# Kernel tuning notes

Hardware: AMD Instinct MI355X
Metric: run time of the kernel (lower is better)

The kernel has to match this reference:

```python
import jax, jax.numpy as jnp
import numpy as np
from jax import lax

LN_EPS = 1e-5
DENOM_EPS = 1e-6


def taylor_exp(x, f):
    # x: [..., f] -> [..., 1 + f + f*f]
    r2 = np.sqrt(2.0).astype(np.float32)
    rd = np.sqrt(float(f)).astype(np.float32)
    rrd = np.sqrt(np.sqrt(float(f))).astype(np.float32)
    x2 = (x[..., :, None] * x[..., None, :]).reshape(*x.shape[:-1], f * f) / r2
    return jnp.concatenate([jnp.ones_like(x[..., :1]), x / rrd, x2 / rd], axis=-1)


def layer_norm(x, gamma, beta):
    mu = jnp.mean(x, axis=-1, keepdims=True)
    var = jnp.mean(jnp.square(x - mu), axis=-1, keepdims=True)
    return (x - mu) * lax.rsqrt(var + LN_EPS) * gamma + beta


def setup_inputs() -> dict:
    key = jax.random.key(0)
    ks = jax.random.split(key, 24)
    B, L, d, h, f, hd, w = 4, 2048, 1024, 16, 16, 64, 64
    D = 1 + f + f * f  # 273

    def lin_w(k, fi, fo):
        return (jax.random.normal(k, (fi, fo), jnp.float32) / np.sqrt(fi)).astype(jnp.float32)

    def lin_b(k, fo):
        return 0.01 * jax.random.normal(k, (fo,), jnp.float32)

    inp = {
        'x': jax.random.normal(ks[0], (B, L, d), jnp.float32),
        'kv_state': jnp.zeros((B, h, D, hd), jnp.float32),
        'k_state': jnp.zeros((B, h, D), jnp.float32),
        'k_buf': jnp.zeros((1, h, w, hd), jnp.float32),
        'v_buf': jnp.zeros((1, h, w, hd), jnp.float32),
        # LinearAttention projections
        'Wq_lin': lin_w(ks[1], d, f * h), 'bq_lin': lin_b(ks[2], f * h),
        'Wk_lin': lin_w(ks[3], d, f * h), 'bk_lin': lin_b(ks[4], f * h),
        'Wv_lin': lin_w(ks[5], d, hd * h), 'bv_lin': lin_b(ks[6], hd * h),
        'Wo_lin': lin_w(ks[7], d, d), 'bo_lin': lin_b(ks[8], d),
        # BasedBlock window-attention projections
        'Wq': lin_w(ks[9], d, d), 'bq': lin_b(ks[10], d),
        'Wk': lin_w(ks[11], d, d), 'bk': lin_b(ks[12], d),
        'Wv': lin_w(ks[13], d, d), 'bv': lin_b(ks[14], d),
        'Wo': lin_w(ks[15], d, d), 'bo': lin_b(ks[16], d),
        # shared LayerNorm
        'gamma': jnp.ones((d,), jnp.float32),
        'beta': jnp.zeros((d,), jnp.float32),
    }
    return inp


def reference(x, kv_state, k_state, k_buf, v_buf,
              Wq_lin, bq_lin, Wk_lin, bk_lin, Wv_lin, bv_lin, Wo_lin, bo_lin,
              Wq, bq, Wk, bk, Wv, bv, Wo, bo, gamma, beta):
    B, L, d = x.shape
    h = kv_state.shape[1]
    hd = kv_state.shape[3]
    f = Wq_lin.shape[1] // h

    # ---- LinearAttention ----
    q = (x @ Wq_lin + bq_lin).reshape(B, L, h, f).transpose(0, 2, 1, 3)   # b h l f
    k = (x @ Wk_lin + bk_lin).reshape(B, L, h, f).transpose(0, 2, 1, 3)
    v = (x @ Wv_lin + bv_lin).reshape(B, L, h, hd).transpose(0, 2, 1, 3)  # b h l hd
    qf = taylor_exp(q, f)  # b h l D
    kf = taylor_exp(k, f)

    # time-major for scan: [l, b, h, ...]
    qt = qf.transpose(2, 0, 1, 3)
    kt = kf.transpose(2, 0, 1, 3)
    vt = v.transpose(2, 0, 1, 3)

    def step(carry, inp):
        kv, kst = carry
        q_t, k_t, v_t = inp
        kv = kv + k_t[..., :, None] * v_t[..., None, :]            # b h D hd
        kst = kst + k_t                                            # b h D
        num = jnp.einsum('bhd,bhdc->bhc', q_t, kv)
        den = jnp.einsum('bhd,bhd->bh', q_t, kst) + DENOM_EPS
        return (kv, kst), num / den[..., None]

    (kv_new, k_new), outs = lax.scan(step, (kv_state, k_state), (qt, kt, vt))
    lin = outs.transpose(1, 0, 2, 3).reshape(B, L, h * hd)  # b l (h hd)
    lin_out = lin @ Wo_lin + bo_lin  # dropout is identity in eval

    x1 = layer_norm(x + lin_out, gamma, beta)

    # ---- window attention ----
    q2 = (x1 @ Wq + bq).reshape(B, L, h, hd).transpose(0, 2, 1, 3)  # b h l hd
    k2 = (x1 @ Wk + bk).reshape(B, L, h, hd).transpose(0, 2, 1, 3)
    v2 = (x1 @ Wv + bv).reshape(B, L, h, hd).transpose(0, 2, 1, 3)

    new_k = k2[:, :, -1:, :]
    new_v = v2[:, :, -1:, :]
    kb = jnp.broadcast_to(k_buf, (B,) + k_buf.shape[1:])
    vb = jnp.broadcast_to(v_buf, (B,) + v_buf.shape[1:])
    uk = jnp.concatenate([kb[:, :, 1:], new_k], axis=2)  # b h w hd
    uv = jnp.concatenate([vb[:, :, 1:], new_v], axis=2)

    scores = jnp.einsum('bhqd,bhwd->bhqw', q2, uk) / np.sqrt(float(hd))
    attn = jax.nn.softmax(scores, axis=-1)
    win = jnp.einsum('bhqw,bhwd->bhqd', attn, uv)
    win = win.transpose(0, 2, 1, 3).reshape(B, L, h * hd)

    out = layer_norm(x1 + (win @ Wo + bo), gamma, beta)
    return out, kv_new, k_new
```

## Files before the change

kernel.cpp:

```cpp
#include <hip/hip_runtime.h>
#include <math.h>


#define LL 2048
#define DD 1024
#define DFEAT 273
#define NC 16
#define CHUNK 128
#define QKVN 1536

typedef __attribute__((ext_vector_type(8))) short short8;
typedef __attribute__((ext_vector_type(4))) float f32x4;

#define SQ 0.42044820762685725f
#define LF 1.18920711500272107f

__device__ __forceinline__ float4 f4(float a, float b, float c, float d) {
  float4 r; r.x = a; r.y = b; r.z = c; r.w = d; return r;
}

__device__ __forceinline__ unsigned short f2bf(float f) {
  union { float f; unsigned u; } v; v.f = f;
  unsigned r = v.u + 0x7fffu + ((v.u >> 16) & 1u);
  return (unsigned short)(r >> 16);
}

__device__ __forceinline__ float bf2f(unsigned short u) {
  union { unsigned u; float f; } v; v.u = ((unsigned)u) << 16; return v.f;
}

__global__ __launch_bounds__(256) void cast_bf16(
    const float* __restrict__ in, unsigned short* __restrict__ o, int n4) {
  int i = blockIdx.x * 256 + threadIdx.x;
  if (i < n4) {
    float4 v = ((const float4*)in)[i];
    ushort4 r;
    r.x = f2bf(v.x); r.y = f2bf(v.y); r.z = f2bf(v.z); r.w = f2bf(v.w);
    ((ushort4*)o)[i] = r;
  }
}

__global__ __launch_bounds__(256) void castT_all(
    const float* __restrict__ Wql, const float* __restrict__ Wkl,
    const float* __restrict__ Wvl, const float* __restrict__ Wo1,
    const float* __restrict__ Wq2, const float* __restrict__ Wo2,
    const float* __restrict__ bql, const float* __restrict__ bkl,
    const float* __restrict__ bvl,
    unsigned short* __restrict__ Wcomb, unsigned short* __restrict__ WtO1,
    unsigned short* __restrict__ WtQ2, unsigned short* __restrict__ WtO2,
    float* __restrict__ bqkv) {
  __shared__ float t[64][65];
  const int blk = blockIdx.x, tid = threadIdx.x;
  if (blk < 6) {
    int i = blk * 256 + tid;
    float v = (i < 256) ? bql[i] : (i < 512) ? bkl[i - 256] : bvl[i - 512];
    bqkv[i] = v;
  }
  const float* W; unsigned short* Wt; int N, t0;
  if (blk < 64)       { W = Wql; Wt = Wcomb;               N = 256;  t0 = blk; }
  else if (blk < 128) { W = Wkl; Wt = Wcomb + 256 * 1024;  N = 256;  t0 = blk - 64; }
  else if (blk < 384) { W = Wvl; Wt = Wcomb + 512 * 1024;  N = 1024; t0 = blk - 128; }
  else if (blk < 640) { W = Wo1; Wt = WtO1;                N = 1024; t0 = blk - 384; }
  else if (blk < 896) { W = Wq2; Wt = WtQ2;                N = 1024; t0 = blk - 640; }
  else                { W = Wo2; Wt = WtO2;                N = 1024; t0 = blk - 896; }
  const int nt = N >> 6;
  const int k0 = (t0 / nt) * 64, n0 = (t0 % nt) * 64;
#pragma unroll
  for (int p = 0; p < 16; p++) {
    int idx = p * 256 + tid;
    int r = idx >> 6, c = idx & 63;
    t[r][c] = W[(size_t)(k0 + r) * N + n0 + c];
  }
  __syncthreads();
#pragma unroll
  for (int p = 0; p < 16; p++) {
    int idx = p * 256 + tid;
    int rn = idx >> 6, ck = idx & 63;
    Wt[(size_t)(n0 + rn) * 1024 + k0 + ck] = f2bf(t[ck][rn]);
  }
}

__global__ __launch_bounds__(256) void gemm_mfma(
    const unsigned short* __restrict__ A, const unsigned short* __restrict__ Bt,
    const float* __restrict__ bias, float* __restrict__ C,
    unsigned short* __restrict__ Cb, int M, int N, int K) {
  __shared__ unsigned short As[128 * 64];
  __shared__ unsigned short Bs[128 * 64];
  const int tid = threadIdx.x;
  const int lane = tid & 63, w = tid >> 6;
  const int row0 = blockIdx.x * 128, col0 = blockIdx.y * 128;
  const int wm0 = (w & 1) * 64, wn0 = (w >> 1) * 64;
  const int lr = lane >> 3;
  const int gc = (lane & 7) ^ lr;
  const unsigned short* aP = A + (size_t)(row0 + w * 32 + lr) * K + gc * 8;
  const unsigned short* bP = Bt + (size_t)(col0 + w * 32 + lr) * K + gc * 8;
  unsigned short* asW = As + w * 2048;
  unsigned short* bsW = Bs + w * 2048;
  const int m15 = lane & 15, quad = lane >> 4;
  f32x4 acc[4][4] = {};
  for (int k0 = 0; k0 < K; k0 += 64) {
#pragma unroll
    for (int i = 0; i < 4; i++) {
      __builtin_amdgcn_global_load_lds(
          (const __attribute__((address_space(1))) unsigned int*)(const void*)(aP + (size_t)(i * 8) * K + k0),
          (__attribute__((address_space(3))) unsigned int*)(void*)(asW + i * 512), 16, 0, 0);
      __builtin_amdgcn_global_load_lds(
          (const __attribute__((address_space(1))) unsigned int*)(const void*)(bP + (size_t)(i * 8) * K + k0),
          (__attribute__((address_space(3))) unsigned int*)(void*)(bsW + i * 512), 16, 0, 0);
    }
    __syncthreads();
#pragma unroll
    for (int ks = 0; ks < 2; ks++) {
      short8 aF[4], bF[4];
#pragma unroll
      for (int mi = 0; mi < 4; mi++) {
        int r = wm0 + mi * 16 + m15;
        int g = (ks * 4 + quad) ^ (r & 7);
        aF[mi] = *(const short8*)(As + r * 64 + g * 8);
      }
#pragma unroll
      for (int ni = 0; ni < 4; ni++) {
        int r = wn0 + ni * 16 + m15;
        int g = (ks * 4 + quad) ^ (r & 7);
        bF[ni] = *(const short8*)(Bs + r * 64 + g * 8);
      }
#pragma unroll
      for (int mi = 0; mi < 4; mi++)
#pragma unroll
        for (int ni = 0; ni < 4; ni++)
          acc[mi][ni] = __builtin_amdgcn_mfma_f32_16x16x32_bf16(
              aF[mi], bF[ni], acc[mi][ni], 0, 0, 0);
    }
    __syncthreads();
  }
#pragma unroll
  for (int mi = 0; mi < 4; mi++)
#pragma unroll
    for (int ni = 0; ni < 4; ni++) {
      int col = col0 + wn0 + ni * 16 + m15;
      float bb = bias[col];
#pragma unroll
      for (int r = 0; r < 4; r++) {
        int row = row0 + wm0 + mi * 16 + quad * 4 + r;
        float val = acc[mi][ni][r] + bb;
        if (Cb) Cb[(size_t)row * N + col] = f2bf(val);
        else C[(size_t)row * N + col] = val;
      }
    }
}

__global__ __launch_bounds__(256) void transV(
    const unsigned short* __restrict__ qkv, unsigned short* __restrict__ vT) {
  __shared__ unsigned short Tv[64][72];
  const int blk = blockIdx.x;
  const int bh = blk >> 5, tt = blk & 31;
  const int b = bh >> 4, hh = bh & 15;
  const int t0 = tt * 64;
  const int tid = threadIdx.x;
  {
    int t = tid >> 2, cs = tid & 3;
    const unsigned short* p = qkv + ((size_t)(b * LL + t0 + t)) * QKVN + 512 + hh * 64 + cs * 16;
    *(short8*)&Tv[t][cs * 16] = *(const short8*)p;
    *(short8*)&Tv[t][cs * 16 + 8] = *(const short8*)(p + 8);
  }
  __syncthreads();
  {
    int c = tid & 63, ts = tid >> 6;
    unsigned short vals[16];
#pragma unroll
    for (int j = 0; j < 16; j++) vals[j] = Tv[ts * 16 + j][c];
    unsigned short* op = vT + ((size_t)bh * 64 + c) * LL + t0 + ts * 16;
    *(short8*)op = *(short8*)&vals[0];
    *(short8*)(op + 8) = *(short8*)&vals[8];
  }
}

__global__ __launch_bounds__(256) void phaseA2(
    const unsigned short* __restrict__ qkv, const unsigned short* __restrict__ vT,
    unsigned short* __restrict__ KVc_t, unsigned short* __restrict__ kstc) {
  __shared__ unsigned short kT[16][136];
  const int tid = threadIdx.x, lane = tid & 63, w = tid >> 6;
  const int m15 = lane & 15, quad = lane >> 4;
  const int bh = blockIdx.x >> 4, ck = blockIdx.x & 15;
  const int b = bh >> 4, hh = bh & 15;
  const int t0 = ck * CHUNK;
  {
    int r = tid >> 1, half = tid & 1;
    short8 kv = *(const short8*)(qkv + ((size_t)(b * LL + t0 + r)) * QKVN + 256 + hh * 16 + half * 8);
#pragma unroll
    for (int j = 0; j < 8; j++)
      kT[half * 8 + j][r] = f2bf(bf2f(((unsigned short*)&kv)[j]) * SQ);
  }
  __syncthreads();
  short8 ones8 = {16256, 16256, 16256, 16256, 16256, 16256, 16256, 16256};
  short8 zer8 = {0, 0, 0, 0, 0, 0, 0, 0};
  f32x4 acc[5][5] = {};
  const unsigned short* vbase = vT + (size_t)bh * 64 * LL + t0;
#pragma unroll
  for (int ks = 0; ks < 4; ++ks) {
    const int tt = ks * 32 + quad * 8;
    short8 aF[5], bF[5];
#pragma unroll
    for (int mi = 0; mi < 5; mi++) {
      int r = (w * 5 + mi) * 16 + m15;
      short8 av;
      unsigned short* pv = (unsigned short*)&av;
      if (r == 0) {
        av = ones8;
      } else if (r < 17) {
        short8 k1 = *(const short8*)&kT[r - 1][tt];
#pragma unroll
        for (int j = 0; j < 8; j++) pv[j] = f2bf(bf2f(((unsigned short*)&k1)[j]) * LF);
      } else if (r < DFEAT) {
        int ij = r - 17;
        short8 k1 = *(const short8*)&kT[ij >> 4][tt];
        short8 k2 = *(const short8*)&kT[ij & 15][tt];
#pragma unroll
        for (int j = 0; j < 8; j++)
          pv[j] = f2bf(bf2f(((unsigned short*)&k1)[j]) * bf2f(((unsigned short*)&k2)[j]));
      } else {
        av = zer8;
      }
      aF[mi] = av;
    }
#pragma unroll
    for (int ni = 0; ni < 4; ni++)
      bF[ni] = *(const short8*)(vbase + ((size_t)(ni * 16 + m15)) * LL + tt);
    bF[4] = (m15 == 0) ? ones8 : zer8;
#pragma unroll
    for (int mi = 0; mi < 5; mi++)
#pragma unroll
      for (int ni = 0; ni < 5; ni++)
        acc[mi][ni] = __builtin_amdgcn_mfma_f32_16x16x32_bf16(
            aF[mi], bF[ni], acc[mi][ni], 0, 0, 0);
  }
  const size_t cb = ((size_t)bh * NC + ck) * (64 * 288);
  const size_t kb = ((size_t)bh * NC + ck) * 288;
#pragma unroll
  for (int mi = 0; mi < 5; mi++) {
    int fb = (w * 5 + mi) * 16 + quad * 4;
    if (fb < 288) {
#pragma unroll
      for (int ni = 0; ni < 4; ni++) {
        int c = ni * 16 + m15;
        ushort4 sv;
        sv.x = f2bf(acc[mi][ni][0]); sv.y = f2bf(acc[mi][ni][1]);
        sv.z = f2bf(acc[mi][ni][2]); sv.w = f2bf(acc[mi][ni][3]);
        *(ushort4*)(KVc_t + cb + (size_t)c * 288 + fb) = sv;
      }
      if (m15 == 0) {
        ushort4 sv;
        sv.x = f2bf(acc[mi][4][0]); sv.y = f2bf(acc[mi][4][1]);
        sv.z = f2bf(acc[mi][4][2]); sv.w = f2bf(acc[mi][4][3]);
        *(ushort4*)(kstc + kb + fb) = sv;
      }
    }
  }
}

__global__ __launch_bounds__(256) void phaseB3(
    const unsigned short* __restrict__ KVc_t, const unsigned short* __restrict__ kstc,
    const float* __restrict__ kv0, const float* __restrict__ kst0,
    unsigned short* __restrict__ KVp_t, unsigned short* __restrict__ kstp,
    float* __restrict__ kv_out, float* __restrict__ kst_out) {
  const int tid = threadIdx.x;
  if (blockIdx.x < 576) {
    int gid = blockIdx.x * 256 + tid;
    int bh = gid / 2304, rem = gid - bh * 2304;
    int c = rem / 36, fg = rem - c * 36;
    int f0 = fg * 8;
    float acc[8];
#pragma unroll
    for (int j = 0; j < 8; j++) {
      int f = f0 + j;
      acc[j] = (f < DFEAT) ? kv0[((size_t)bh * DFEAT + f) * 64 + c] : 0.0f;
    }
    size_t base = ((size_t)bh * NC) * (64 * 288) + (size_t)c * 288 + f0;
    for (int ck = 0; ck < NC; ck++) {
      size_t idx = base + (size_t)ck * (64 * 288);
      short8 t = *(const short8*)(KVc_t + idx);
      unsigned short ov[8];
#pragma unroll
      for (int j = 0; j < 8; j++) {
        ov[j] = f2bf(acc[j]);
        acc[j] += bf2f(((unsigned short*)&t)[j]);
      }
      *(short8*)(KVp_t + idx) = *(short8*)ov;
    }
#pragma unroll
    for (int j = 0; j < 8; j++) {
      int f = f0 + j;
      if (f < DFEAT) kv_out[((size_t)bh * DFEAT + f) * 64 + c] = acc[j];
    }
  } else {
    int idx0 = (blockIdx.x - 576) * 256 + tid;
    int bh = idx0 / 36, fg = idx0 - bh * 36;
    int f0 = fg * 8;
    float acc[8];
#pragma unroll
    for (int j = 0; j < 8; j++) {
      int f = f0 + j;
      acc[j] = (f < DFEAT) ? kst0[bh * DFEAT + f] : 0.0f;
    }
    for (int ck = 0; ck < NC; ck++) {
      size_t idx = ((size_t)bh * NC + ck) * 288 + f0;
      short8 t = *(const short8*)(kstc + idx);
      unsigned short ov[8];
#pragma unroll
      for (int j = 0; j < 8; j++) {
        ov[j] = f2bf(acc[j]);
        acc[j] += bf2f(((unsigned short*)&t)[j]);
      }
      *(short8*)(kstp + idx) = *(short8*)ov;
    }
#pragma unroll
    for (int j = 0; j < 8; j++) {
      int f = f0 + j;
      if (f < DFEAT) kst_out[bh * DFEAT + f] = acc[j];
    }
  }
}

__global__ __launch_bounds__(256) void phaseC4(
    const unsigned short* __restrict__ qkv,
    const unsigned short* __restrict__ vT, const unsigned short* __restrict__ KVp_t,
    const unsigned short* __restrict__ kstp, unsigned short* __restrict__ outs) {
  __shared__ float qs[4][32][36];
  __shared__ unsigned short S_l[4][32 * 128];
  const int tid = threadIdx.x, lane = tid & 63, w = tid >> 6;
  const int m15 = lane & 15, quad = lane >> 4;
  const int bh = blockIdx.x >> 4, ck = blockIdx.x & 15;
  const int qw = w;
  const int b = bh >> 4, hh = bh & 15;
  const int t0 = ck * CHUNK;
  const int tr0 = qw * 32;
  float (*qsw)[36] = qs[w];
  unsigned short* Sw = S_l[w];
  const unsigned short* qbase = qkv + ((size_t)(b * LL + t0 + tr0)) * QKVN + hh * 16;
  const unsigned short* kbase = qkv + ((size_t)(b * LL + t0)) * QKVN + 256 + hh * 16;
  {
    int r = lane >> 1, h8 = lane & 1;
    short8 qv = *(const short8*)(qbase + (size_t)r * QKVN + h8 * 8);
    float qf[8];
#pragma unroll
    for (int j = 0; j < 8; j++) qf[j] = bf2f(((unsigned short*)&qv)[j]) * SQ;
    *(float4*)&qsw[r][h8 * 8] = f4(qf[0], qf[1], qf[2], qf[3]);
    *(float4*)&qsw[r][h8 * 8 + 4] = f4(qf[4], qf[5], qf[6], qf[7]);
#pragma unroll
    for (int j = 0; j < 8; j++)
      qsw[r][16 + ((h8 * 8 + j + 9) & 15)] = qf[j];
  }
  short8 ones8 = {16256, 16256, 16256, 16256, 16256, 16256, 16256, 16256};
  short8 zer8 = {0, 0, 0, 0, 0, 0, 0, 0};
  f32x4 acc[2][5] = {};
  const unsigned short* KVb = KVp_t + ((size_t)(bh * NC + ck)) * (64 * 288);
  const unsigned short* kstb = kstp + ((size_t)(bh * NC + ck)) * 288;
#pragma unroll
  for (int ks = 0; ks < 9; ++ks) {
    const int fs = ks * 32 + quad * 8;
    short8 aF[2], bF[5];
#pragma unroll
    for (int ni = 0; ni < 4; ni++)
      bF[ni] = *(const short8*)(KVb + ((size_t)(ni * 16 + m15)) * 288 + fs);
    bF[4] = (m15 == 0) ? *(const short8*)(kstb + fs) : zer8;
#pragma unroll
    for (int mi = 0; mi < 2; mi++) {
      const float* qr = &qsw[mi * 16 + m15][0];
      unsigned short pv[8];
      if (ks == 0) {
        float qr0 = qr[0];
#pragma unroll
        for (int j = 0; j < 8; j++) {
          int f = (quad << 3) + j;
          int fl = f - 1; fl = fl < 0 ? 0 : fl;
          int fm = f - 17; fm = fm < 0 ? 0 : fm;
          float lin = qr[fl] * LF;
          float prod = qr0 * qr[fm];
          float val = (f == 0) ? 1.0f : ((f < 17) ? lin : prod);
          pv[j] = f2bf(val);
        }
      } else {
        int base = fs - 17;
        int i0 = base >> 4;
        float qi0 = qr[i0];
        float qi1 = qr[i0 + 1];
        const float* qv = qr + 16 + (base & 8);
        float qj[8];
        *(float4*)&qj[0] = *(const float4*)qv;
        *(float4*)&qj[4] = *(const float4*)(qv + 4);
        float qiB = (quad & 1) ? qi0 : qi1;
#pragma unroll
        for (int j = 0; j < 8; j++) {
          float qi = (j == 0) ? qi0 : qiB;
          float val = qi * qj[j];
          if (ks == 8) val = ((quad << 3) + j < 17) ? val : 0.0f;
          pv[j] = f2bf(val);
        }
      }
      aF[mi] = *(short8*)pv;
    }
#pragma unroll
    for (int mi = 0; mi < 2; mi++)
#pragma unroll
      for (int ni = 0; ni < 5; ni++)
        acc[mi][ni] = __builtin_amdgcn_mfma_f32_16x16x32_bf16(
            aF[mi], bF[ni], acc[mi][ni], 0, 0, 0);
  }
  const int nsn = 2 * qw + 2;
  {
    short8 aU[2], bU[8];
    aU[0] = (quad < 2) ? *(const short8*)(qbase + (size_t)m15 * QKVN + quad * 8) : zer8;
    aU[1] = (quad < 2) ? *(const short8*)(qbase + (size_t)(16 + m15) * QKVN + quad * 8) : zer8;
#pragma unroll
    for (int sn = 0; sn < 8; sn++) {
      if (sn < nsn) {
        int s = sn * 16 + m15;
        bU[sn] = (quad < 2) ? *(const short8*)(kbase + (size_t)s * QKVN + quad * 8) : zer8;
      }
    }
#pragma unroll
    for (int mi = 0; mi < 2; mi++) {
#pragma unroll
      for (int sn = 0; sn < 8; sn++) {
        if (sn < nsn) {
          f32x4 zz = {0.f, 0.f, 0.f, 0.f};
          f32x4 u = __builtin_amdgcn_mfma_f32_16x16x32_bf16(aU[mi], bU[sn], zz, 0, 0, 0);
          int s = sn * 16 + m15;
          int gRow = s >> 3;
#pragma unroll
          for (int rr = 0; rr < 4; rr++) {
            int tl = mi * 16 + quad * 4 + rr;
            int tc = tr0 + tl;
            float uu = u[rr];
            float sv = (s <= tc) ? fmaf(uu, fmaf(uu, 0.03125f, 0.25f), 1.0f) : 0.0f;
            int p = gRow ^ (tl & 7);
            Sw[tl * 128 + p * 8 + (s & 7)] = f2bf(sv);
          }
        }
      }
    }
  }
  const unsigned short* vbase = vT + (size_t)bh * 64 * LL + t0;
#pragma unroll
  for (int ks = 0; ks < 4; ++ks) {
    if (ks <= qw) {
      const int tt = ks * 32 + quad * 8;
      short8 aF[2], bF[5];
#pragma unroll
      for (int mi = 0; mi < 2; mi++) {
        int tl = mi * 16 + m15;
        int p = (ks * 4 + quad) ^ (tl & 7);
        aF[mi] = *(const short8*)&Sw[tl * 128 + p * 8];
      }
#pragma unroll
      for (int ni = 0; ni < 4; ni++)
        bF[ni] = *(const short8*)(vbase + ((size_t)(ni * 16 + m15)) * LL + tt);
      bF[4] = (m15 == 0) ? ones8 : zer8;
#pragma unroll
      for (int mi = 0; mi < 2; mi++)
#pragma unroll
        for (int ni = 0; ni < 5; ni++)
          acc[mi][ni] = __builtin_amdgcn_mfma_f32_16x16x32_bf16(
              aF[mi], bF[ni], acc[mi][ni], 0, 0, 0);
    }
  }
#pragma unroll
  for (int mi = 0; mi < 2; mi++) {
#pragma unroll
    for (int rr = 0; rr < 4; rr++) {
      float den = __shfl(acc[mi][4][rr], (lane & 48));
      float inv = 1.0f / (den + 1e-6f);
      int tl = mi * 16 + quad * 4 + rr;
      unsigned short* op = outs + ((size_t)(b * LL + t0 + tr0 + tl)) * DD + hh * 64;
#pragma unroll
      for (int ni = 0; ni < 4; ni++)
        op[ni * 16 + m15] = f2bf(acc[mi][ni][rr] * inv);
    }
  }
}

__global__ __launch_bounds__(256) void lastrow_init(
    const float* __restrict__ bk, const float* __restrict__ bv,
    float* __restrict__ klast, float* __restrict__ vlast) {
  int gid = blockIdx.x * 256 + threadIdx.x;
  int which = gid >> 12;
  int b = (gid >> 10) & 3;
  int n = gid & 1023;
  (which ? vlast : klast)[b * 1024 + n] = which ? bv[n] : bk[n];
}

__global__ __launch_bounds__(256) void lastrow_qkv2(
    const unsigned short* __restrict__ x1b,
    const float* __restrict__ Wk, const float* __restrict__ Wv,
    float* __restrict__ klast, float* __restrict__ vlast) {
  __shared__ float xs[4][64];
  __shared__ float red[4][4][64];
  const int blk = blockIdx.x;
  const int which = blk >> 8;
  const int nstrip = (blk >> 4) & 15;
  const int kslice = blk & 15;
  const int n0 = nstrip * 64, k0 = kslice * 64;
  const int tid = threadIdx.x;
  const int nn = tid & 63, p = tid >> 6;
  {
    int b = tid >> 6, k = tid & 63;
    xs[b][k] = bf2f(x1b[((size_t)(b * LL + LL - 1)) * DD + k0 + k]);
  }
  __syncthreads();
  const float* W = which ? Wv : Wk;
  float acc[4] = {};
#pragma unroll
  for (int i = 0; i < 16; i++) {
    int kk = p * 16 + i;
    float wv = W[(size_t)(k0 + kk) * 1024 + n0 + nn];
#pragma unroll
    for (int b = 0; b < 4; b++) acc[b] = fmaf(xs[b][kk], wv, acc[b]);
  }
#pragma unroll
  for (int b = 0; b < 4; b++) red[p][b][nn] = acc[b];
  __syncthreads();
  if (p == 0) {
    float* outp = which ? vlast : klast;
#pragma unroll
    for (int b = 0; b < 4; b++) {
      float s = red[0][b][nn] + red[1][b][nn] + red[2][b][nn] + red[3][b][nn];
      atomicAdd(outp + b * 1024 + n0 + nn, s);
    }
  }
}

__global__ __launch_bounds__(256) void prep_window(
    const float* __restrict__ kbuf, const float* __restrict__ vbufw,
    const float* __restrict__ klast, const float* __restrict__ vlast,
    unsigned short* __restrict__ ukb, unsigned short* __restrict__ uvT) {
  __shared__ float Tv[64][68];
  const int bh = blockIdx.x;
  const int b = bh >> 4, hh = bh & 15;
  const int tid = threadIdx.x;
  const int wi = tid >> 2, d0 = (tid & 3) * 16;
  {
    const float* kp = (wi < 63) ? (kbuf + ((size_t)hh * 64 + wi + 1) * 64 + d0)
                                : (klast + (size_t)b * 1024 + hh * 64 + d0);
    unsigned short* op = ukb + ((size_t)bh * 64 + wi) * 64 + d0;
#pragma unroll
    for (int j4 = 0; j4 < 4; j4++) {
      float4 v = *(const float4*)(kp + j4 * 4);
      ushort4 r;
      r.x = f2bf(v.x); r.y = f2bf(v.y); r.z = f2bf(v.z); r.w = f2bf(v.w);
      *(ushort4*)(op + j4 * 4) = r;
    }
  }
  {
    const float* vp = (wi < 63) ? (vbufw + ((size_t)hh * 64 + wi + 1) * 64 + d0)
                                : (vlast + (size_t)b * 1024 + hh * 64 + d0);
#pragma unroll
    for (int j4 = 0; j4 < 4; j4++)
      *(float4*)&Tv[wi][d0 + j4 * 4] = *(const float4*)(vp + j4 * 4);
  }
  __syncthreads();
  {
    int c = tid & 63, w0 = (tid >> 6) * 16;
    unsigned short* op = uvT + ((size_t)bh * 64 + c) * 64 + w0;
    unsigned short vals[16];
#pragma unroll
    for (int j = 0; j < 16; j++) vals[j] = f2bf(Tv[w0 + j][c]);
    *(short8*)op = *(short8*)&vals[0];
    *(short8*)(op + 8) = *(short8*)&vals[8];
  }
}

__global__ __launch_bounds__(256) void window_attn2(
    const unsigned short* __restrict__ q2b, const unsigned short* __restrict__ ukb,
    const unsigned short* __restrict__ uvT, unsigned short* __restrict__ win) {
  __shared__ unsigned short S_l[128 * 64];
  const int tid = threadIdx.x, lane = tid & 63, w = tid >> 6;
  const int m15 = lane & 15, quad = lane >> 4;
  const int bh = blockIdx.x >> 4, tile = blockIdx.x & 15;
  const int b = bh >> 4, hh = bh & 15;
  const int t0 = tile * 128 + w * 32;
  const unsigned short* ukbase = ukb + (size_t)bh * 64 * 64;
  const unsigned short* uvbase = uvT + (size_t)bh * 64 * 64;
  f32x4 accS[2][4] = {};
#pragma unroll
  for (int ks = 0; ks < 2; ks++) {
    short8 aF[2], bF[4];
#pragma unroll
    for (int mi = 0; mi < 2; mi++)
      aF[mi] = *(const short8*)(q2b + ((size_t)(b * LL + t0 + mi * 16 + m15)) * DD +
                                hh * 64 + ks * 32 + quad * 8);
#pragma unroll
    for (int ni = 0; ni < 4; ni++)
      bF[ni] = *(const short8*)(ukbase + ((size_t)(ni * 16 + m15)) * 64 + ks * 32 + quad * 8);
#pragma unroll
    for (int mi = 0; mi < 2; mi++)
#pragma unroll
      for (int ni = 0; ni < 4; ni++)
        accS[mi][ni] = __builtin_amdgcn_mfma_f32_16x16x32_bf16(
            aF[mi], bF[ni], accS[mi][ni], 0, 0, 0);
  }
#pragma unroll
  for (int mi = 0; mi < 2; mi++) {
#pragma unroll
    for (int rr = 0; rr < 4; rr++) {
      float s0 = accS[mi][0][rr] * 0.125f;
      float s1 = accS[mi][1][rr] * 0.125f;
      float s2 = accS[mi][2][rr] * 0.125f;
      float s3 = accS[mi][3][rr] * 0.125f;
      float m = fmaxf(fmaxf(s0, s1), fmaxf(s2, s3));
      m = fmaxf(m, __shfl_xor(m, 1));
      m = fmaxf(m, __shfl_xor(m, 2));
      m = fmaxf(m, __shfl_xor(m, 4));
      m = fmaxf(m, __shfl_xor(m, 8));
      float p0 = __expf(s0 - m), p1 = __expf(s1 - m);
      float p2 = __expf(s2 - m), p3 = __expf(s3 - m);
      float l = p0 + p1 + p2 + p3;
      l += __shfl_xor(l, 1);
      l += __shfl_xor(l, 2);
      l += __shfl_xor(l, 4);
      l += __shfl_xor(l, 8);
      float inv = 1.0f / l;
      int tl = w * 32 + mi * 16 + quad * 4 + rr;
      int t7 = tl & 7;
      float pr[4] = {p0 * inv, p1 * inv, p2 * inv, p3 * inv};
#pragma unroll
      for (int ni = 0; ni < 4; ni++) {
        int s = ni * 16 + m15;
        S_l[tl * 64 + ((s >> 3) ^ t7) * 8 + (s & 7)] = f2bf(pr[ni]);
      }
    }
  }
  f32x4 accO[2][4] = {};
#pragma unroll
  for (int ks = 0; ks < 2; ks++) {
    short8 aF[2], bF[4];
#pragma unroll
    for (int mi = 0; mi < 2; mi++) {
      int tl = w * 32 + mi * 16 + m15;
      int g = (ks * 4 + quad) ^ (tl & 7);
      aF[mi] = *(const short8*)&S_l[tl * 64 + g * 8];
    }
#pragma unroll
    for (int ni = 0; ni < 4; ni++)
      bF[ni] = *(const short8*)(uvbase + ((size_t)(ni * 16 + m15)) * 64 + ks * 32 + quad * 8);
#pragma unroll
    for (int mi = 0; mi < 2; mi++)
#pragma unroll
      for (int ni = 0; ni < 4; ni++)
        accO[mi][ni] = __builtin_amdgcn_mfma_f32_16x16x32_bf16(
            aF[mi], bF[ni], accO[mi][ni], 0, 0, 0);
  }
#pragma unroll
  for (int mi = 0; mi < 2; mi++) {
#pragma unroll
    for (int rr = 0; rr < 4; rr++) {
      int row = t0 + mi * 16 + quad * 4 + rr;
      unsigned short* op = win + ((size_t)(b * LL + row)) * DD + hh * 64;
#pragma unroll
      for (int ni = 0; ni < 4; ni++)
        op[ni * 16 + m15] = f2bf(accO[mi][ni][rr]);
    }
  }
}

__global__ __launch_bounds__(256) void ln_add2(
    const float* __restrict__ Af, const unsigned short* __restrict__ Ab,
    const unsigned short* __restrict__ Bmb,
    const float* __restrict__ gamma, const float* __restrict__ beta,
    float* __restrict__ out, unsigned short* __restrict__ outb) {
  const int row = blockIdx.x, tid = threadIdx.x;
  float a0, a1, a2, a3;
  if (Af) {
    float4 va = ((const float4*)(Af + (size_t)row * DD))[tid];
    a0 = va.x; a1 = va.y; a2 = va.z; a3 = va.w;
  } else {
    ushort4 ua = ((const ushort4*)(Ab + (size_t)row * DD))[tid];
    a0 = bf2f(ua.x); a1 = bf2f(ua.y); a2 = bf2f(ua.z); a3 = bf2f(ua.w);
  }
  ushort4 ub = ((const ushort4*)(Bmb + (size_t)row * DD))[tid];
  float4 s4 = f4(a0 + bf2f(ub.x), a1 + bf2f(ub.y), a2 + bf2f(ub.z), a3 + bf2f(ub.w));
  float s = s4.x + s4.y + s4.z + s4.w;
  float ss = s4.x * s4.x + s4.y * s4.y + s4.z * s4.z + s4.w * s4.w;
  for (int o = 32; o; o >>= 1) { s += __shfl_xor(s, o); ss += __shfl_xor(ss, o); }
  __shared__ float red[8];
  int wid = tid >> 6;
  if ((tid & 63) == 0) { red[wid * 2] = s; red[wid * 2 + 1] = ss; }
  __syncthreads();
  float tot = red[0] + red[2] + red[4] + red[6];
  float tots = red[1] + red[3] + red[5] + red[7];
  float mu = tot * (1.0f / 1024.0f);
  float var = tots * (1.0f / 1024.0f) - mu * mu;
  float rstd = rsqrtf(var + 1e-5f);
  float4 g = ((const float4*)gamma)[tid];
  float4 be = ((const float4*)beta)[tid];
  float4 o = f4((s4.x - mu) * rstd * g.x + be.x, (s4.y - mu) * rstd * g.y + be.y,
                (s4.z - mu) * rstd * g.z + be.z, (s4.w - mu) * rstd * g.w + be.w);
  if (out) ((float4*)(out + (size_t)row * DD))[tid] = o;
  if (outb) {
    ushort4 r;
    r.x = f2bf(o.x); r.y = f2bf(o.y); r.z = f2bf(o.z); r.w = f2bf(o.w);
    ((ushort4*)(outb + (size_t)row * DD))[tid] = r;
  }
}

extern "C" void kernel_launch(void* const* d_in, const int* in_sizes, int n_in,
                              void* d_out, int out_size, void* d_ws, size_t ws_size,
                              hipStream_t stream) {
  (void)in_sizes; (void)n_in; (void)out_size; (void)ws_size;
  const float* x      = (const float*)d_in[0];
  const float* kv0    = (const float*)d_in[1];
  const float* kst0   = (const float*)d_in[2];
  const float* kbuf   = (const float*)d_in[3];
  const float* vbufw  = (const float*)d_in[4];
  const float* Wq_lin = (const float*)d_in[5];
  const float* bq_lin = (const float*)d_in[6];
  const float* Wk_lin = (const float*)d_in[7];
  const float* bk_lin = (const float*)d_in[8];
  const float* Wv_lin = (const float*)d_in[9];
  const float* bv_lin = (const float*)d_in[10];
  const float* Wo_lin = (const float*)d_in[11];
  const float* bo_lin = (const float*)d_in[12];
  const float* Wq     = (const float*)d_in[13];
  const float* bq     = (const float*)d_in[14];
  const float* Wk     = (const float*)d_in[15];
  const float* bk     = (const float*)d_in[16];
  const float* Wv     = (const float*)d_in[17];
  const float* bv     = (const float*)d_in[18];
  const float* Wo     = (const float*)d_in[19];
  const float* bo     = (const float*)d_in[20];
  const float* gamma  = (const float*)d_in[21];
  const float* beta   = (const float*)d_in[22];

  float* out = (float*)d_out;
  float* kv_out  = out + 8388608;
  float* kst_out = out + 8388608 + 1118208;

  float* ws = (float*)d_ws;
  const size_t MF = 1024 * 1024;
  unsigned short* x_bf   = (unsigned short*)(ws);
  unsigned short* qkv_b  = (unsigned short*)(ws + 4 * MF);
  unsigned short* vT     = (unsigned short*)(ws + 10 * MF);
  unsigned short* KVc_t  = (unsigned short*)(ws + 14 * MF);
  unsigned short* kstc   = (unsigned short*)(ws + 23 * MF);
  unsigned short* KVp_t  = (unsigned short*)(ws + 24 * MF);
  unsigned short* kstp   = (unsigned short*)(ws + 33 * MF);
  unsigned short* outs_bf = (unsigned short*)(ws + 34 * MF);
  unsigned short* tmp_b  = (unsigned short*)(ws + 38 * MF);
  unsigned short* x1b    = (unsigned short*)(ws + 42 * MF);
  unsigned short* q2b    = (unsigned short*)(ws + 46 * MF);
  unsigned short* winb   = (unsigned short*)(ws + 50 * MF);
  unsigned short* tmp2_b = (unsigned short*)(ws + 54 * MF);
  float* klast = ws + 58 * MF;
  float* vlast = klast + 4096;
  unsigned short* ukb  = (unsigned short*)(ws + 58 * MF + 8192);
  unsigned short* uvTw = ukb + 262144;
  unsigned short* Wcomb = (unsigned short*)(ws + 59 * MF);
  unsigned short* WtO1  = (unsigned short*)(ws + 60 * MF);
  unsigned short* WtQ2  = (unsigned short*)(ws + 61 * MF);
  unsigned short* WtO2  = (unsigned short*)(ws + 62 * MF);
  float* bqkv = ws + 63 * MF;

  dim3 blk(256);
  cast_bf16<<<8192, blk, 0, stream>>>(x, x_bf, 2097152);
  castT_all<<<1152, blk, 0, stream>>>(Wq_lin, Wk_lin, Wv_lin, Wo_lin, Wq, Wo,
                                      bq_lin, bk_lin, bv_lin,
                                      Wcomb, WtO1, WtQ2, WtO2, bqkv);
  gemm_mfma<<<dim3(64, 12), blk, 0, stream>>>(x_bf, Wcomb, bqkv, (float*)0, qkv_b, 8192, QKVN, 1024);
  transV<<<2048, blk, 0, stream>>>(qkv_b, vT);
  phaseA2<<<1024, blk, 0, stream>>>(qkv_b, vT, KVc_t, kstc);
  phaseB3<<<585, blk, 0, stream>>>(KVc_t, kstc, kv0, kst0, KVp_t, kstp, kv_out, kst_out);
  phaseC4<<<1024, blk, 0, stream>>>(qkv_b, vT, KVp_t, kstp, outs_bf);
  gemm_mfma<<<dim3(64, 8), blk, 0, stream>>>(outs_bf, WtO1, bo_lin, (float*)0, tmp_b, 8192, 1024, 1024);
  ln_add2<<<8192, blk, 0, stream>>>(x, (const unsigned short*)0, tmp_b, gamma, beta, (float*)0, x1b);
  gemm_mfma<<<dim3(64, 8), blk, 0, stream>>>(x1b, WtQ2, bq, (float*)0, q2b, 8192, 1024, 1024);
  lastrow_init<<<32, blk, 0, stream>>>(bk, bv, klast, vlast);
  lastrow_qkv2<<<512, blk, 0, stream>>>(x1b, Wk, Wv, klast, vlast);
  prep_window<<<64, blk, 0, stream>>>(kbuf, vbufw, klast, vlast, ukb, uvTw);
  window_attn2<<<1024, blk, 0, stream>>>(q2b, ukb, uvTw, winb);
  gemm_mfma<<<dim3(64, 8), blk, 0, stream>>>(winb, WtO2, bo, (float*)0, tmp2_b, 8192, 1024, 1024);
  ln_add2<<<8192, blk, 0, stream>>>((const float*)0, x1b, tmp2_b, gamma, beta, out, (unsigned short*)0);
}
```

Before: 388.9 us.

## Merge prep kernels and remap block IDs for XCD-aware locality

Folds the x cast, the weight transpose-casts and the lastrow bias init into one prep launch, so two kernel launches go away. The GEMM moves to a 1D grid and, like phaseA2 and phaseC4, remaps block IDs so that blocks landing on the same XCD (round-robin by blockIdx mod 8) handle neighbouring tiles. This should improve L2 reuse of shared A/B rows and chunk data. The cost is extra index arithmetic, plus a remap that assumes the grid size is divisible by 8.

```diff
diff --git a/kernel.cpp b/kernel.cpp
--- a/kernel.cpp
+++ b/kernel.cpp
@@ -29,18 +29,8 @@
   union { unsigned u; float f; } v; v.u = ((unsigned)u) << 16; return v.f;
 }
 
-__global__ __launch_bounds__(256) void cast_bf16(
-    const float* __restrict__ in, unsigned short* __restrict__ o, int n4) {
-  int i = blockIdx.x * 256 + threadIdx.x;
-  if (i < n4) {
-    float4 v = ((const float4*)in)[i];
-    ushort4 r;
-    r.x = f2bf(v.x); r.y = f2bf(v.y); r.z = f2bf(v.z); r.w = f2bf(v.w);
-    ((ushort4*)o)[i] = r;
-  }
-}
-
-__global__ __launch_bounds__(256) void castT_all(
+__global__ __launch_bounds__(256) void prep_all(
+    const float* __restrict__ x, unsigned short* __restrict__ x_bf,
     const float* __restrict__ Wql, const float* __restrict__ Wkl,
     const float* __restrict__ Wvl, const float* __restrict__ Wo1,
     const float* __restrict__ Wq2, const float* __restrict__ Wo2,
@@ -48,21 +38,40 @@
     const float* __restrict__ bvl,
     unsigned short* __restrict__ Wcomb, unsigned short* __restrict__ WtO1,
     unsigned short* __restrict__ WtQ2, unsigned short* __restrict__ WtO2,
-    float* __restrict__ bqkv) {
+    float* __restrict__ bqkv,
+    const float* __restrict__ bk, const float* __restrict__ bv,
+    float* __restrict__ klast, float* __restrict__ vlast) {
   __shared__ float t[64][65];
   const int blk = blockIdx.x, tid = threadIdx.x;
-  if (blk < 6) {
+  if (blk < 8192) {
     int i = blk * 256 + tid;
+    float4 v = ((const float4*)x)[i];
+    ushort4 r;
+    r.x = f2bf(v.x); r.y = f2bf(v.y); r.z = f2bf(v.z); r.w = f2bf(v.w);
+    ((ushort4*)x_bf)[i] = r;
+    return;
+  }
+  if (blk >= 9344) {
+    int gid = (blk - 9344) * 256 + tid;
+    int which = gid >> 12;
+    int b = (gid >> 10) & 3;
+    int n = gid & 1023;
+    (which ? vlast : klast)[b * 1024 + n] = which ? bv[n] : bk[n];
+    return;
+  }
+  const int b2 = blk - 8192;
+  if (b2 < 6) {
+    int i = b2 * 256 + tid;
     float v = (i < 256) ? bql[i] : (i < 512) ? bkl[i - 256] : bvl[i - 512];
     bqkv[i] = v;
   }
   const float* W; unsigned short* Wt; int N, t0;
-  if (blk < 64)       { W = Wql; Wt = Wcomb;               N = 256;  t0 = blk; }
-  else if (blk < 128) { W = Wkl; Wt = Wcomb + 256 * 1024;  N = 256;  t0 = blk - 64; }
-  else if (blk < 384) { W = Wvl; Wt = Wcomb + 512 * 1024;  N = 1024; t0 = blk - 128; }
-  else if (blk < 640) { W = Wo1; Wt = WtO1;                N = 1024; t0 = blk - 384; }
-  else if (blk < 896) { W = Wq2; Wt = WtQ2;                N = 1024; t0 = blk - 640; }
-  else                { W = Wo2; Wt = WtO2;                N = 1024; t0 = blk - 896; }
+  if (b2 < 64)       { W = Wql; Wt = Wcomb;               N = 256;  t0 = b2; }
+  else if (b2 < 128) { W = Wkl; Wt = Wcomb + 256 * 1024;  N = 256;  t0 = b2 - 64; }
+  else if (b2 < 384) { W = Wvl; Wt = Wcomb + 512 * 1024;  N = 1024; t0 = b2 - 128; }
+  else if (b2 < 640) { W = Wo1; Wt = WtO1;                N = 1024; t0 = b2 - 384; }
+  else if (b2 < 896) { W = Wq2; Wt = WtQ2;                N = 1024; t0 = b2 - 640; }
+  else               { W = Wo2; Wt = WtO2;                N = 1024; t0 = b2 - 896; }
   const int nt = N >> 6;
   const int k0 = (t0 / nt) * 64, n0 = (t0 % nt) * 64;
 #pragma unroll
@@ -88,7 +97,12 @@
   __shared__ unsigned short Bs[128 * 64];
   const int tid = threadIdx.x;
   const int lane = tid & 63, w = tid >> 6;
-  const int row0 = blockIdx.x * 128, col0 = blockIdx.y * 128;
+  const int Ny = N >> 7;
+  const int cpx = gridDim.x >> 3;
+  const int orig = blockIdx.x;
+  const int wg = (orig & 7) * cpx + (orig >> 3);
+  const int bxi = wg / Ny, byi = wg - bxi * Ny;
+  const int row0 = bxi * 128, col0 = byi * 128;
   const int wm0 = (w & 1) * 64, wn0 = (w >> 1) * 64;
   const int lr = lane >> 3;
   const int gc = (lane & 7) ^ lr;
@@ -181,7 +195,9 @@
   __shared__ unsigned short kT[16][136];
   const int tid = threadIdx.x, lane = tid & 63, w = tid >> 6;
   const int m15 = lane & 15, quad = lane >> 4;
-  const int bh = blockIdx.x >> 4, ck = blockIdx.x & 15;
+  const int orig = blockIdx.x;
+  const int wg = (orig & 7) * 128 + (orig >> 3);
+  const int bh = wg >> 4, ck = wg & 15;
   const int b = bh >> 4, hh = bh & 15;
   const int t0 = ck * CHUNK;
   {
@@ -329,7 +345,9 @@
   __shared__ unsigned short S_l[4][32 * 128];
   const int tid = threadIdx.x, lane = tid & 63, w = tid >> 6;
   const int m15 = lane & 15, quad = lane >> 4;
-  const int bh = blockIdx.x >> 4, ck = blockIdx.x & 15;
+  const int orig = blockIdx.x;
+  const int wgb = (orig & 7) * 128 + (orig >> 3);
+  const int bh = wgb >> 4, ck = wgb & 15;
   const int qw = w;
   const int b = bh >> 4, hh = bh & 15;
   const int t0 = ck * CHUNK;
@@ -477,16 +495,6 @@
         op[ni * 16 + m15] = f2bf(acc[mi][ni][rr] * inv);
     }
   }
-}
-
-__global__ __launch_bounds__(256) void lastrow_init(
-    const float* __restrict__ bk, const float* __restrict__ bv,
-    float* __restrict__ klast, float* __restrict__ vlast) {
-  int gid = blockIdx.x * 256 + threadIdx.x;
-  int which = gid >> 12;
-  int b = (gid >> 10) & 3;
-  int n = gid & 1023;
-  (which ? vlast : klast)[b * 1024 + n] = which ? bv[n] : bk[n];
 }
 
 __global__ __launch_bounds__(256) void lastrow_qkv2(
@@ -760,22 +768,22 @@
   float* bqkv = ws + 63 * MF;
 
   dim3 blk(256);
-  cast_bf16<<<8192, blk, 0, stream>>>(x, x_bf, 2097152);
-  castT_all<<<1152, blk, 0, stream>>>(Wq_lin, Wk_lin, Wv_lin, Wo_lin, Wq, Wo,
-                                      bq_lin, bk_lin, bv_lin,
-                                      Wcomb, WtO1, WtQ2, WtO2, bqkv);
-  gemm_mfma<<<dim3(64, 12), blk, 0, stream>>>(x_bf, Wcomb, bqkv, (float*)0, qkv_b, 8192, QKVN, 1024);
+  prep_all<<<9376, blk, 0, stream>>>(x, x_bf,
+                                     Wq_lin, Wk_lin, Wv_lin, Wo_lin, Wq, Wo,
+                                     bq_lin, bk_lin, bv_lin,
+                                     Wcomb, WtO1, WtQ2, WtO2, bqkv,
+                                     bk, bv, klast, vlast);
+  gemm_mfma<<<768, blk, 0, stream>>>(x_bf, Wcomb, bqkv, (float*)0, qkv_b, 8192, QKVN, 1024);
   transV<<<2048, blk, 0, stream>>>(qkv_b, vT);
   phaseA2<<<1024, blk, 0, stream>>>(qkv_b, vT, KVc_t, kstc);
   phaseB3<<<585, blk, 0, stream>>>(KVc_t, kstc, kv0, kst0, KVp_t, kstp, kv_out, kst_out);
   phaseC4<<<1024, blk, 0, stream>>>(qkv_b, vT, KVp_t, kstp, outs_bf);
-  gemm_mfma<<<dim3(64, 8), blk, 0, stream>>>(outs_bf, WtO1, bo_lin, (float*)0, tmp_b, 8192, 1024, 1024);
+  gemm_mfma<<<512, blk, 0, stream>>>(outs_bf, WtO1, bo_lin, (float*)0, tmp_b, 8192, 1024, 1024);
   ln_add2<<<8192, blk, 0, stream>>>(x, (const unsigned short*)0, tmp_b, gamma, beta, (float*)0, x1b);
-  gemm_mfma<<<dim3(64, 8), blk, 0, stream>>>(x1b, WtQ2, bq, (float*)0, q2b, 8192, 1024, 1024);
-  lastrow_init<<<32, blk, 0, stream>>>(bk, bv, klast, vlast);
+  gemm_mfma<<<512, blk, 0, stream>>>(x1b, WtQ2, bq, (float*)0, q2b, 8192, 1024, 1024);
   lastrow_qkv2<<<512, blk, 0, stream>>>(x1b, Wk, Wv, klast, vlast);
   prep_window<<<64, blk, 0, stream>>>(kbuf, vbufw, klast, vlast, ukb, uvTw);
   window_attn2<<<1024, blk, 0, stream>>>(q2b, ukb, uvTw, winb);
-  gemm_mfma<<<dim3(64, 8), blk, 0, stream>>>(winb, WtO2, bo, (float*)0, tmp2_b, 8192, 1024, 1024);
+  gemm_mfma<<<512, blk, 0, stream>>>(winb, WtO2, bo, (float*)0, tmp2_b, 8192, 1024, 1024);
   ln_add2<<<8192, blk, 0, stream>>>((const float*)0, x1b, tmp2_b, gamma, beta, out, (unsigned short*)0);
 }
```

Measured after the change: 383.8 us. No clear change (-1.3%).
